# Kernel tuning notes

Measured on AMD Instinct MI355X. Metric: run time of the kernel, lower is better.

The kernel has to match this reference:

```python
import jax, jax.numpy as jnp
import numpy as np

B, T, C = 2, 2048, 1024
H = 16
D = C // H
E = 16
K = 2
THETA = 10000.0
ALPHA = 0.01
EPS = 1e-5


def rmsnorm(x, w):
    ms = jnp.mean(jnp.square(x), axis=-1, keepdims=True)
    return x * jax.lax.rsqrt(ms + EPS) * w


def rope_cos_sin(t_len, dim):
    # matches precompute_freqs_cis: freqs = theta**(-2i/dim), angles = t * freqs
    freqs = 1.0 / THETA ** (jnp.arange(0, dim // 2, dtype=jnp.float32) * 2.0 / dim)
    ang = jnp.arange(t_len, dtype=jnp.float32)[:, None] * freqs[None, :]  # [T, D/2]
    return jnp.cos(ang), jnp.sin(ang)


def apply_rope(x, cos, sin):
    # x: [B,T,H,D]; complex rotation on consecutive pairs (view_as_complex semantics)
    xr = x.reshape(x.shape[:-1] + (D // 2, 2))
    x0, x1 = xr[..., 0], xr[..., 1]
    c = cos[None, :, None, :]
    s = sin[None, :, None, :]
    return jnp.stack([x0 * c - x1 * s, x0 * s + x1 * c], axis=-1).reshape(x.shape)


def mlp(x, wf, bf, wp, bp):
    return jax.nn.silu(x @ wf + bf) @ wp + bp


def setup_inputs() -> dict:
    key = jax.random.key(0)
    ks = jax.random.split(key, 16)
    s = 0.02
    return {
        'x': jax.random.normal(ks[0], (B, T, C), jnp.float32),
        'ln1_w': jax.random.normal(ks[1], (C,), jnp.float32),
        'ln2_w': jax.random.normal(ks[2], (C,), jnp.float32),
        'w_attn': jax.random.normal(ks[3], (C, 3 * C), jnp.float32) * s,
        'b_attn': jnp.zeros((3 * C,), jnp.float32),
        'w_proj': jax.random.normal(ks[4], (C, C), jnp.float32) * s,
        'b_proj': jnp.zeros((C,), jnp.float32),
        'gate_w': jax.random.normal(ks[5], (E, C), jnp.float32) * s,
        'gate_bias': jnp.zeros((E,), jnp.float32),
        'exp_wf': jax.random.normal(ks[6], (E, C, 2 * C), jnp.float32) * s,
        'exp_bf': jnp.zeros((E, 2 * C), jnp.float32),
        'exp_wp': jax.random.normal(ks[7], (E, 2 * C, C), jnp.float32) * s,
        'exp_bp': jnp.zeros((E, C), jnp.float32),
        'sh_wf': jax.random.normal(ks[8], (C, 2 * C), jnp.float32) * s,
        'sh_bf': jnp.zeros((2 * C,), jnp.float32),
        'sh_wp': jax.random.normal(ks[9], (2 * C, C), jnp.float32) * s,
        'sh_bp': jnp.zeros((C,), jnp.float32),
    }


def reference(x, ln1_w, ln2_w, w_attn, b_attn, w_proj, b_proj, gate_w, gate_bias,
              exp_wf, exp_bf, exp_wp, exp_bp, sh_wf, sh_bf, sh_wp, sh_bp):
    # ---- attention sub-block ----
    h = rmsnorm(x, ln1_w)
    qkv = h @ w_attn + b_attn  # [B,T,3C]
    q, k, v = jnp.split(qkv, 3, axis=-1)
    q = q.reshape(B, T, H, D)
    k = k.reshape(B, T, H, D)
    v = v.reshape(B, T, H, D)
    cos, sin = rope_cos_sin(T, D)
    q = apply_rope(q, cos, sin)
    k = apply_rope(k, cos, sin)
    scores = jnp.einsum('bqhd,bkhd->bhqk', q, k) / jnp.sqrt(jnp.float32(D))
    causal = jnp.tril(jnp.ones((T, T), dtype=bool))
    scores = jnp.where(causal, scores, -jnp.inf)
    attn = jax.nn.softmax(scores, axis=-1)
    y = jnp.einsum('bhqk,bkhd->bqhd', attn, v).reshape(B, T, C)
    x = x + y @ w_proj + b_proj
    # ---- MoE sub-block ----
    h = rmsnorm(x, ln2_w).reshape(-1, C)  # [N,C]
    N = h.shape[0]
    logits = h @ gate_w.T
    p = jax.nn.softmax(logits.astype(jnp.float32), axis=-1)  # original_scores [N,E]
    _, idx = jax.lax.top_k(p + gate_bias, K)  # topk on biased scores
    w_sel = jnp.take_along_axis(p, idx, axis=-1)  # weights from unbiased scores [N,K]
    onehot = jax.nn.one_hot(idx, E, dtype=p.dtype)  # [N,K,E]
    w_dense = jnp.sum(onehot * w_sel[..., None], axis=1)  # [N,E] combine weights
    counts = jnp.sum(onehot, axis=(0, 1))  # bincount
    f_i = counts * E / (K * N + 1e-6)
    expert_probs = p.mean(axis=0)
    lb_loss = ALPHA * jnp.sum(f_i * expert_probs)
    out = jnp.zeros_like(h)
    for i in range(E):  # fixed small expert count
        out = out + mlp(h, exp_wf[i], exp_bf[i], exp_wp[i], exp_bp[i]) * w_dense[:, i:i + 1]
    out = out + mlp(h, sh_wf, sh_bf, sh_wp, sh_bp)
    return x + out.reshape(B, T, C), lb_loss
```

## Files before the change

### kernel.cpp

```cpp
#include <hip/hip_runtime.h>

typedef __bf16 bf16x8 __attribute__((ext_vector_type(8)));
typedef short  short8 __attribute__((ext_vector_type(8)));
typedef float  f32x4  __attribute__((ext_vector_type(4)));
typedef unsigned short u16;

#define NTOK 4096
#define TSEQ 2048
#define CDIM 1024
#define NEXP 16

__device__ __forceinline__ u16 f2bf(float f){
  union { float f; unsigned u; } v; v.f = f;
  unsigned r = v.u + 0x7fffu + ((v.u >> 16) & 1u);
  return (u16)(r >> 16);
}
__device__ __forceinline__ float bf2f(u16 u){
  union { unsigned u; float f; } v; v.u = ((unsigned)u) << 16; return v.f;
}

__device__ __forceinline__ f32x4 mfma16(short8 a, short8 b, f32x4 c){
  return __builtin_amdgcn_mfma_f32_16x16x32_bf16(
      __builtin_bit_cast(bf16x8, a), __builtin_bit_cast(bf16x8, b), c, 0, 0, 0);
}

__device__ __forceinline__ void gload_lds16(const void* g, void* l){
  __builtin_amdgcn_global_load_lds((__attribute__((address_space(1))) void*)g,
                                   (__attribute__((address_space(3))) void*)l,
                                   16, 0, 0);
}

__device__ __forceinline__ void tp_body(const float* __restrict__ in, u16* __restrict__ out,
                                        int K, int N, int k0, int n0, u16* lds16, int tid)
{
  int tx = tid & 15;
#pragma unroll
  for (int p = 0; p < 2; ++p) {
    int q = (tid >> 4) + p * 16;
    int k = 2 * q;
    float4 v0 = *(const float4*)(in + (size_t)(k0 + k)     * N + n0 + tx * 4);
    float4 v1 = *(const float4*)(in + (size_t)(k0 + k + 1) * N + n0 + tx * 4);
    const float* a0 = (const float*)&v0;
    const float* a1 = (const float*)&v1;
#pragma unroll
    for (int i = 0; i < 4; ++i) {
      unsigned val = (unsigned)f2bf(a0[i]) | ((unsigned)f2bf(a1[i]) << 16);
      *(unsigned*)&lds16[(tx * 4 + i) * 66 + k] = val;
    }
  }
  __syncthreads();
#pragma unroll
  for (int p = 0; p < 2; ++p) {
    int n = (tid >> 3) + p * 32;
    int k8 = (tid & 7) * 8;
    const unsigned* l32 = (const unsigned*)&lds16[n * 66 + k8];
    uint4 o4;
    o4.x = l32[0]; o4.y = l32[1]; o4.z = l32[2]; o4.w = l32[3];
    *(uint4*)(out + (size_t)(n0 + n) * K + k0 + k8) = o4;
  }
}

__global__ void transpose_wattn_k(const float* __restrict__ in, u16* __restrict__ out)
{
  __shared__ u16 lds16[64 * 66];
  int r = blockIdx.x;
  int n0 = (r % 48) * 64, k0 = (r / 48) * 64;
  tp_body(in, out, 1024, 3072, k0, n0, lds16, threadIdx.x);
}

__global__ void concat_bias_k(const float* __restrict__ exp_bf, const float* __restrict__ sh_bf,
                              const float* __restrict__ exp_bp, const float* __restrict__ sh_bp,
                              float* __restrict__ bf17, float* __restrict__ bp17,
                              int* __restrict__ counts)
{
  int i = blockIdx.x * 256 + threadIdx.x;
  if (i < 16 * 2048) bf17[i] = exp_bf[i];
  else if (i < 17 * 2048) bf17[i] = sh_bf[i - 16 * 2048];
  if (i < 16 * 1024) bp17[i] = exp_bp[i];
  else if (i < 17 * 1024) bp17[i] = sh_bp[i - 16 * 1024];
  if (blockIdx.x == 0 && threadIdx.x <= NEXP)
    counts[threadIdx.x] = (threadIdx.x == NEXP) ? NTOK : 0;
}

__global__ void rmsnorm_k(const float* __restrict__ x, const float* __restrict__ w,
                          u16* __restrict__ ob)
{
  int row = blockIdx.x, tid = threadIdx.x;
  const float4* xr = (const float4*)(x + (size_t)row * CDIM);
  float4 v = xr[tid];
  float ss = v.x*v.x + v.y*v.y + v.z*v.z + v.w*v.w;
  for (int d = 1; d < 64; d <<= 1) ss += __shfl_xor(ss, d);
  __shared__ float wacc[4];
  if ((tid & 63) == 0) wacc[tid >> 6] = ss;
  __syncthreads();
  float tot = wacc[0] + wacc[1] + wacc[2] + wacc[3];
  float scale = rsqrtf(tot * (1.0f / CDIM) + 1e-5f);
  float4 wv = ((const float4*)w)[tid];
  float o0 = v.x * scale * wv.x, o1 = v.y * scale * wv.y;
  float o2 = v.z * scale * wv.z, o3 = v.w * scale * wv.w;
  ushort4 ov; ov.x = f2bf(o0); ov.y = f2bf(o1); ov.z = f2bf(o2); ov.w = f2bf(o3);
  ((ushort4*)(ob + (size_t)row * CDIM))[tid] = ov;
}

__global__ void rmsnorm_gate_k(const float* __restrict__ x2, const float* __restrict__ w,
                               const float* __restrict__ gw, const float* __restrict__ gb,
                               u16* __restrict__ ob,
                               int* __restrict__ route_e, float* __restrict__ route_w,
                               int* __restrict__ counts, float* __restrict__ probs)
{
  int row = blockIdx.x, tid = threadIdx.x;
  __shared__ float hrow[CDIM];
  __shared__ float wacc[4];
  __shared__ float part[16][17];
  __shared__ float sm[16];

  const float4* xr = (const float4*)(x2 + (size_t)row * CDIM);
  float4 v = xr[tid];
  float ss = v.x*v.x + v.y*v.y + v.z*v.z + v.w*v.w;
  for (int d = 1; d < 64; d <<= 1) ss += __shfl_xor(ss, d);
  if ((tid & 63) == 0) wacc[tid >> 6] = ss;
  __syncthreads();
  float tot = wacc[0] + wacc[1] + wacc[2] + wacc[3];
  float scale = rsqrtf(tot * (1.0f / CDIM) + 1e-5f);
  float4 wv = ((const float4*)w)[tid];
  float o0 = v.x * scale * wv.x, o1 = v.y * scale * wv.y;
  float o2 = v.z * scale * wv.z, o3 = v.w * scale * wv.w;
  ((float4*)hrow)[tid] = make_float4(o0, o1, o2, o3);
  ushort4 ov; ov.x = f2bf(o0); ov.y = f2bf(o1); ov.z = f2bf(o2); ov.w = f2bf(o3);
  ((ushort4*)(ob + (size_t)row * CDIM))[tid] = ov;
  __syncthreads();

  int e = tid & 15, seg = tid >> 4;
  const float4* gw4 = (const float4*)(gw + (size_t)e * CDIM + seg * 64);
  const float4* hs4 = (const float4*)(hrow + seg * 64);
  float p = 0.f;
#pragma unroll
  for (int i = 0; i < 16; ++i) {
    float4 gv = gw4[i];
    float4 hv = hs4[i];
    p += hv.x * gv.x;
    p += hv.y * gv.y;
    p += hv.z * gv.z;
    p += hv.w * gv.w;
  }
  part[e][seg] = p;
  __syncthreads();
  if (tid < 16) {
    float lg = 0.f;
    for (int s = 0; s < 16; ++s) lg += part[tid][s];
    sm[tid] = lg;
  }
  __syncthreads();
  if (tid == 0) {
    float mx = sm[0];
    for (int i = 1; i < 16; ++i) mx = fmaxf(mx, sm[i]);
    float ssum = 0.f;
    for (int i = 0; i < 16; ++i) { float pe = expf(sm[i] - mx); sm[i] = pe; ssum += pe; }
    float inv = 1.0f / ssum;
    for (int i = 0; i < 16; ++i) sm[i] *= inv;
    int i1 = -1; float b1 = -1e30f;
    for (int i = 0; i < 16; ++i) { float t = sm[i] + gb[i]; if (t > b1) { b1 = t; i1 = i; } }
    int i2 = -1; float b2 = -1e30f;
    for (int i = 0; i < 16; ++i) { if (i == i1) continue; float t = sm[i] + gb[i]; if (t > b2) { b2 = t; i2 = i; } }
    route_e[2 * row] = i1; route_e[2 * row + 1] = i2;
    route_w[2 * row] = sm[i1]; route_w[2 * row + 1] = sm[i2];
    atomicAdd(&counts[i1], 1); atomicAdd(&counts[i2], 1);
  }
  __syncthreads();
  if (tid < 16) probs[(size_t)row * 16 + tid] = sm[tid];
}

template<int MODE, int SWZ>
__global__ void __launch_bounds__(256, 4)
gemm_bt(const u16* __restrict__ A, int lda,
        const u16* __restrict__ Bt, long long bStrideZ,
        const float* __restrict__ bias, int biasStrideZ,
        void* __restrict__ Cout,
        const float* __restrict__ resid,
        int M, int N, int K,
        const int* __restrict__ counts, const int* __restrict__ offsets,
        const int* __restrict__ tokA, u16* __restrict__ vtp)
{
  int cb, rb, z;
  if (SWZ) {
    int nwg = gridDim.x * gridDim.y * gridDim.z;
    int d = (blockIdx.z * gridDim.y + blockIdx.y) * gridDim.x + blockIdx.x;
    int o = (d & 7) * (nwg >> 3) + (d >> 3);
    cb = o % gridDim.x;
    int t2 = o / gridDim.x;
    rb = t2 % gridDim.y;
    z  = t2 / gridDim.y;
  } else {
    cb = blockIdx.x; rb = blockIdx.y; z = blockIdx.z;
  }

  int mLoc = M, rowBase = 0;
  if (counts) { mLoc = counts[z]; rowBase = offsets[z]; }
  if (rb * 128 >= mLoc) return;

  const u16* Bz = Bt + (size_t)z * bStrideZ;
  const float* bz = bias + (size_t)z * biasStrideZ;

  __shared__ u16 lds_a[2][128 * 32];
  __shared__ u16 lds_b[2][128 * 32];

  int tid = threadIdx.x;
  int lane = tid & 63, wave = tid >> 6;
  int wm = wave >> 1, wn = wave & 1;
  int srow = wave * 16 + (lane >> 2);
  int skel = (lane & 3) * 8;
  int r16 = lane & 15, g8 = (lane >> 4) * 8;

  size_t arow[2];
  int ncol[2];
#pragma unroll
  for (int c = 0; c < 2; ++c) {
    int rloc = rb * 128 + c * 64 + srow;
    if (rloc >= mLoc) rloc = mLoc - 1;
    int grow = rowBase + rloc;
    arow[c] = tokA ? (size_t)tokA[grow] : (size_t)grow;
    ncol[c] = cb * 128 + c * 64 + srow;
  }

  f32x4 acc[4][4] = {};

  auto stage = [&](int kt, int buf){
    int k0 = kt * 32;
#pragma unroll
    for (int c = 0; c < 2; ++c) {
      gload_lds16(A + arow[c] * lda + k0 + skel,
                  (char*)&lds_a[buf][0] + c * 4096 + wave * 1024);
      gload_lds16(Bz + (size_t)ncol[c] * K + k0 + skel,
                  (char*)&lds_b[buf][0] + c * 4096 + wave * 1024);
    }
  };

  int nkt = K >> 5;
  stage(0, 0);
  for (int kt = 0; kt < nkt; ++kt) {
    int buf = kt & 1;
    if (kt + 1 < nkt) {
      stage(kt + 1, buf ^ 1);
      asm volatile("s_waitcnt vmcnt(4)" ::: "memory");
    } else {
      asm volatile("s_waitcnt vmcnt(0)" ::: "memory");
    }
    __builtin_amdgcn_s_barrier();
    short8 af[4], bfr[4];
#pragma unroll
    for (int i = 0; i < 4; ++i) {
      af[i]  = *(const short8*)&lds_a[buf][(wm * 64 + i * 16 + r16) * 32 + g8];
      bfr[i] = *(const short8*)&lds_b[buf][(wn * 64 + i * 16 + r16) * 32 + g8];
    }
#pragma unroll
    for (int i = 0; i < 4; ++i)
#pragma unroll
      for (int j = 0; j < 4; ++j)
        acc[i][j] = mfma16(af[i], bfr[j], acc[i][j]);
    __builtin_amdgcn_s_barrier();
  }

#pragma unroll
  for (int i = 0; i < 4; ++i) {
    int rl0 = rb * 128 + wm * 64 + i * 16 + (lane >> 4) * 4;
#pragma unroll
    for (int j = 0; j < 4; ++j) {
      int col = cb * 128 + wn * 64 + j * 16 + r16;
      float bv = bz[col];
#pragma unroll
      for (int r = 0; r < 4; ++r) {
        int rl = rl0 + r;
        if (rl >= mLoc) continue;
        int grow = rowBase + rl;
        float v = acc[i][j][r] + bv;
        if (MODE == 0) {
          ((float*)Cout)[(size_t)grow * N + col] = v;
        } else if (MODE == 1) {
          ((float*)Cout)[(size_t)grow * N + col] = v + resid[(size_t)grow * N + col];
        } else if (MODE == 2) {
          float s = v * (1.0f / (1.0f + __expf(-v)));
          ((u16*)Cout)[(size_t)grow * N + col] = f2bf(s);
        } else if (MODE == 4) {
          ((u16*)Cout)[(size_t)grow * N + col] = f2bf(v);
        } else {
          if (col < 2048) {
            ((float*)Cout)[(size_t)grow * N + col] = v;
          } else {
            int c10 = col - 2048;
            int h = c10 >> 6, dd = c10 & 63;
            int b = grow >> 11, t = grow & 2047;
            vtp[((size_t)(b * 16 + h) * 64 + dd) * TSEQ + t] = f2bf(v);
          }
        }
      }
    }
  }
}

__global__ void __launch_bounds__(256, 4)
ff_tp_k(const u16* __restrict__ A, const u16* __restrict__ Wf17,
        const float* __restrict__ bf17, u16* __restrict__ hid17,
        const int* __restrict__ counts, const int* __restrict__ offsets,
        const int* __restrict__ tokA,
        const float* __restrict__ expWp, u16* __restrict__ oWp17)
{
  __shared__ union {
    struct { u16 a[2][128 * 32]; u16 b[2][128 * 32]; } g;
    u16 t[64 * 66];
  } sm;

  int u = blockIdx.x;
  if (u >= 8704) {
    int t = u - 8704;
    int z = t >> 9, r = t & 511;
    tp_body(expWp + (size_t)z * 2048 * 1024, oWp17 + (size_t)z * 2048 * 1024,
            2048, 1024, (r >> 4) * 64, (r & 15) * 64, sm.t, threadIdx.x);
    return;
  }

  const int N = 2048, K = 1024, lda = 1024;
  int cb = u & 15, t2 = u >> 4;
  int rb = t2 & 31, z = t2 >> 5;

  int mLoc = counts[z], rowBase = offsets[z];
  if (rb * 128 >= mLoc) return;

  const u16* Bz = Wf17 + (size_t)z * 2048 * 1024;
  const float* bz = bf17 + (size_t)z * 2048;

  int tid = threadIdx.x;
  int lane = tid & 63, wave = tid >> 6;
  int wm = wave >> 1, wn = wave & 1;
  int srow = wave * 16 + (lane >> 2);
  int skel = (lane & 3) * 8;
  int r16 = lane & 15, g8 = (lane >> 4) * 8;

  size_t arow[2];
  int ncol[2];
#pragma unroll
  for (int c = 0; c < 2; ++c) {
    int rloc = rb * 128 + c * 64 + srow;
    if (rloc >= mLoc) rloc = mLoc - 1;
    int grow = rowBase + rloc;
    arow[c] = (size_t)tokA[grow];
    ncol[c] = cb * 128 + c * 64 + srow;
  }

  f32x4 acc[4][4] = {};

  auto stage = [&](int kt, int buf){
    int k0 = kt * 32;
#pragma unroll
    for (int c = 0; c < 2; ++c) {
      gload_lds16(A + arow[c] * lda + k0 + skel,
                  (char*)&sm.g.a[buf][0] + c * 4096 + wave * 1024);
      gload_lds16(Bz + (size_t)ncol[c] * K + k0 + skel,
                  (char*)&sm.g.b[buf][0] + c * 4096 + wave * 1024);
    }
  };

  int nkt = K >> 5;
  stage(0, 0);
  for (int kt = 0; kt < nkt; ++kt) {
    int buf = kt & 1;
    if (kt + 1 < nkt) {
      stage(kt + 1, buf ^ 1);
      asm volatile("s_waitcnt vmcnt(4)" ::: "memory");
    } else {
      asm volatile("s_waitcnt vmcnt(0)" ::: "memory");
    }
    __builtin_amdgcn_s_barrier();
    short8 af[4], bfr[4];
#pragma unroll
    for (int i = 0; i < 4; ++i) {
      af[i]  = *(const short8*)&sm.g.a[buf][(wm * 64 + i * 16 + r16) * 32 + g8];
      bfr[i] = *(const short8*)&sm.g.b[buf][(wn * 64 + i * 16 + r16) * 32 + g8];
    }
#pragma unroll
    for (int i = 0; i < 4; ++i)
#pragma unroll
      for (int j = 0; j < 4; ++j)
        acc[i][j] = mfma16(af[i], bfr[j], acc[i][j]);
    __builtin_amdgcn_s_barrier();
  }

#pragma unroll
  for (int i = 0; i < 4; ++i) {
    int rl0 = rb * 128 + wm * 64 + i * 16 + (lane >> 4) * 4;
#pragma unroll
    for (int j = 0; j < 4; ++j) {
      int col = cb * 128 + wn * 64 + j * 16 + r16;
      float bv = bz[col];
#pragma unroll
      for (int r = 0; r < 4; ++r) {
        int rl = rl0 + r;
        if (rl >= mLoc) continue;
        int grow = rowBase + rl;
        float v = acc[i][j][r] + bv;
        float s = v * (1.0f / (1.0f + __expf(-v)));
        hid17[(size_t)grow * N + col] = f2bf(s);
      }
    }
  }
}

__global__ void __launch_bounds__(512, 4)
attn_tp_k(const u16* __restrict__ qr, const u16* __restrict__ kr,
          const u16* __restrict__ vt, u16* __restrict__ y,
          const float* __restrict__ wProj, const float* __restrict__ shWf,
          const float* __restrict__ shWp,  const float* __restrict__ expWf,
          u16* __restrict__ oProj, u16* __restrict__ oWf17, u16* __restrict__ oWp17)
{
  __shared__ union {
    struct { u16 lK[2][64 * 64]; u16 lV[2][64 * 64]; u16 plds[8][16 * 72]; } a;
    u16 t[2][64 * 66];
  } sm;

  int u = blockIdx.x;
  if (u >= 512) {
    int tid = threadIdx.x;
    int half = tid >> 8, t256 = tid & 255;
    int t = (u - 512) * 2 + half;
    const float* in; u16* out; int K, N, k0, n0;
    if (t < 8192) {
      int z = t >> 9, r = t & 511;
      in = expWf + (size_t)z * 2048 * 1024; out = oWf17 + (size_t)z * 2048 * 1024;
      K = 1024; N = 2048; n0 = (r & 31) * 64; k0 = (r >> 5) * 64;
    } else if (t < 8704) {
      int r = t - 8192;
      in = shWf; out = oWf17 + (size_t)16 * 2048 * 1024;
      K = 1024; N = 2048; n0 = (r & 31) * 64; k0 = (r >> 5) * 64;
    } else if (t < 9216) {
      int r = t - 8704;
      in = shWp; out = oWp17 + (size_t)16 * 2048 * 1024;
      K = 2048; N = 1024; n0 = (r & 15) * 64; k0 = (r >> 4) * 64;
    } else {
      int r = t - 9216;
      in = wProj; out = oProj; K = 1024; N = 1024; n0 = (r & 15) * 64; k0 = (r >> 4) * 64;
    }
    tp_body(in, out, K, N, k0, n0, &sm.t[half][0], t256);
    return;
  }

  int j  = u >> 5;
  int bh = u & 31;
  int b = bh >> 4, h = bh & 15;
  int qb = 15 - j;
  int tid = threadIdx.x;
  int wv = tid >> 6, lane = tid & 63;
  int qrow0 = qb * 128 + wv * 16;
  const u16* qbase = qr + (size_t)bh * TSEQ * 64;
  const u16* kbase = kr + (size_t)bh * TSEQ * 64;
  const u16* vbase = vt + (size_t)bh * 64 * TSEQ;

  u16* pw = &sm.a.plds[wv][0];

  int r16 = lane & 15, g = lane >> 4;

  short8 aq0 = *(const short8*)(qbase + (size_t)(qrow0 + r16) * 64 + g * 8);
  short8 aq1 = *(const short8*)(qbase + (size_t)(qrow0 + r16) * 64 + 32 + g * 8);

  int sRow = tid >> 3;
  int sColE = (((tid & 7) * 16) ^ ((sRow & 7) << 4)) >> 1;

  float m[4] = {-1e30f, -1e30f, -1e30f, -1e30f};
  float l[4] = {0.f, 0.f, 0.f, 0.f};
  f32x4 o[4] = {};

  int nt = 2 * qb + 2;

  auto stage = [&](int t, int buf){
    int kp = t * 64;
    gload_lds16(kbase + ((size_t)(kp + sRow) << 6) + sColE,
                (char*)&sm.a.lK[buf][0] + wv * 1024);
    gload_lds16(vbase + (size_t)sRow * TSEQ + kp + sColE,
                (char*)&sm.a.lV[buf][0] + wv * 1024);
  };

  auto compute = [&](int t, int buf){
    int kp = t * 64;
    f32x4 s[4];
    __builtin_amdgcn_s_setprio(1);
#pragma unroll
    for (int st = 0; st < 4; ++st) {
      int rowK = st * 16 + r16;
      int sw = (rowK & 7) << 4;
      short8 kb0 = *(const short8*)((const char*)&sm.a.lK[buf][0] + rowK * 128 + ((g * 16) ^ sw));
      short8 kb1 = *(const short8*)((const char*)&sm.a.lK[buf][0] + rowK * 128 + ((64 + g * 16) ^ sw));
      f32x4 acc = {0.f, 0.f, 0.f, 0.f};
      acc = mfma16(aq0, kb0, acc);
      acc = mfma16(aq1, kb1, acc);
      s[st] = acc;
    }
    __builtin_amdgcn_s_setprio(0);

    float sc[4];
#pragma unroll
    for (int r = 0; r < 4; ++r) {
      int qpos = qrow0 + g * 4 + r;
      float v0 = (kp + r16      <= qpos) ? s[0][r] * 0.125f : -1e30f;
      float v1 = (kp + 16 + r16 <= qpos) ? s[1][r] * 0.125f : -1e30f;
      float v2 = (kp + 32 + r16 <= qpos) ? s[2][r] * 0.125f : -1e30f;
      float v3 = (kp + 48 + r16 <= qpos) ? s[3][r] * 0.125f : -1e30f;
      float mx = fmaxf(fmaxf(v0, v1), fmaxf(v2, v3));
      for (int d = 1; d < 16; d <<= 1) mx = fmaxf(mx, __shfl_xor(mx, d));
      float mnew = fmaxf(m[r], mx);
      float e0 = __expf(v0 - mnew), e1 = __expf(v1 - mnew);
      float e2 = __expf(v2 - mnew), e3 = __expf(v3 - mnew);
      float scale = __expf(m[r] - mnew);
      float rs = (e0 + e1) + (e2 + e3);
      for (int d = 1; d < 16; d <<= 1) rs += __shfl_xor(rs, d);
      l[r] = l[r] * scale + rs;
      m[r] = mnew;
      sc[r] = scale;
      int prow = (g * 4 + r) * 72;
      pw[prow + r16]      = f2bf(e0);
      pw[prow + 16 + r16] = f2bf(e1);
      pw[prow + 32 + r16] = f2bf(e2);
      pw[prow + 48 + r16] = f2bf(e3);
    }
#pragma unroll
    for (int c = 0; c < 4; ++c) {
      f32x4 t4 = o[c];
      t4[0] *= sc[0]; t4[1] *= sc[1]; t4[2] *= sc[2]; t4[3] *= sc[3];
      o[c] = t4;
    }

    short8 pa0 = *(const short8*)&pw[r16 * 72 + g * 8];
    short8 pa1 = *(const short8*)&pw[r16 * 72 + 32 + g * 8];
    __builtin_amdgcn_s_setprio(1);
#pragma unroll
    for (int c = 0; c < 4; ++c) {
      int rowV = c * 16 + r16;
      int sw = (rowV & 7) << 4;
      short8 vb0 = *(const short8*)((const char*)&sm.a.lV[buf][0] + rowV * 128 + ((g * 16) ^ sw));
      short8 vb1 = *(const short8*)((const char*)&sm.a.lV[buf][0] + rowV * 128 + ((64 + g * 16) ^ sw));
      o[c] = mfma16(pa0, vb0, o[c]);
      o[c] = mfma16(pa1, vb1, o[c]);
    }
    __builtin_amdgcn_s_setprio(0);
  };

  stage(0, 0);
  for (int t = 0; t < nt; ++t) {
    int buf = t & 1;
    if (t + 1 < nt) {
      stage(t + 1, buf ^ 1);
      asm volatile("s_waitcnt vmcnt(2)" ::: "memory");
    } else {
      asm volatile("s_waitcnt vmcnt(0)" ::: "memory");
    }
    __builtin_amdgcn_s_barrier();
    compute(t, buf);
    __builtin_amdgcn_s_barrier();
  }

#pragma unroll
  for (int c = 0; c < 4; ++c)
#pragma unroll
    for (int r = 0; r < 4; ++r) {
      int qpos = qrow0 + g * 4 + r;
      float val = o[c][r] / l[r];
      y[((size_t)(b * TSEQ + qpos)) * CDIM + h * 64 + c * 16 + r16] = f2bf(val);
    }
}

__global__ void rope_qk_k(const float* __restrict__ qkv,
                          u16* __restrict__ qr, u16* __restrict__ kr)
{
  int flat = blockIdx.x * 256 + threadIdx.x;
  int i = flat & 31;
  int h = (flat >> 5) & 15;
  int n = flat >> 9;
  int b = n >> 11, t = n & 2047;
  const float* row = qkv + (size_t)n * 3072;
  float2 q = *(const float2*)(row + h * 64 + 2 * i);
  float2 k = *(const float2*)(row + 1024 + h * 64 + 2 * i);
  float freq = expf(-(float)i * (2.0f / 64.0f) * 9.210340371976184f);
  float ang = (float)t * freq;
  float sn, cs;
  sincosf(ang, &sn, &cs);
  float q0 = q.x * cs - q.y * sn, q1 = q.x * sn + q.y * cs;
  float k0 = k.x * cs - k.y * sn, k1 = k.x * sn + k.y * cs;
  int bh = b * 16 + h;
  size_t qoff = ((size_t)bh * TSEQ + t) * 64 + 2 * i;
  *(unsigned*)(qr + qoff) = (unsigned)f2bf(q0) | ((unsigned)f2bf(q1) << 16);
  *(unsigned*)(kr + qoff) = (unsigned)f2bf(k0) | ((unsigned)f2bf(k1) << 16);
}

__global__ void route_fin_k(const int* __restrict__ route_e, const float* __restrict__ route_w,
                            const int* __restrict__ counts, int* __restrict__ offs,
                            int* __restrict__ tok, float* __restrict__ tw, int* __restrict__ inv,
                            const float* __restrict__ probs, float* __restrict__ loss_out)
{
  __shared__ int curs[16];
  __shared__ float part[256][16];
  __shared__ float colsum[16];
  int tid = threadIdx.x;
  if (tid == 0) {
    int acc = 0;
    for (int e = 0; e < NEXP; ++e) { offs[e] = acc; curs[e] = acc; acc += counts[e]; }
    offs[NEXP] = acc;
  }
  __syncthreads();
  for (int n = tid; n < NTOK; n += 1024) {
    for (int j = 0; j < 2; ++j) {
      int e = route_e[2 * n + j];
      int pos = atomicAdd(&curs[e], 1);
      tok[pos] = n; tw[pos] = route_w[2 * n + j];
      inv[2 * n + j] = pos;
    }
    tok[2 * NTOK + n] = n;
  }
  __syncthreads();
  if (tid < 256) {
    float acc[16];
#pragma unroll
    for (int e = 0; e < 16; ++e) acc[e] = 0.f;
    for (int n = tid; n < NTOK; n += 256) {
      const float4* row = (const float4*)(probs + (size_t)n * 16);
      float4 a0 = row[0], a1 = row[1], a2 = row[2], a3 = row[3];
      acc[0] += a0.x; acc[1] += a0.y; acc[2]  += a0.z; acc[3]  += a0.w;
      acc[4] += a1.x; acc[5] += a1.y; acc[6]  += a1.z; acc[7]  += a1.w;
      acc[8] += a2.x; acc[9] += a2.y; acc[10] += a2.z; acc[11] += a2.w;
      acc[12] += a3.x; acc[13] += a3.y; acc[14] += a3.z; acc[15] += a3.w;
    }
#pragma unroll
    for (int e = 0; e < 16; ++e) part[tid][e] = acc[e];
  }
  __syncthreads();
  if (tid < 16) {
    float s = 0.f;
    for (int i = 0; i < 256; ++i) s += part[i][tid];
    colsum[tid] = s;
  }
  __syncthreads();
  if (tid == 0) {
    float accl = 0.f;
    for (int e = 0; e < NEXP; ++e) {
      float f = (float)counts[e] * (16.0f / (2.0f * (float)NTOK + 1e-6f));
      accl += f * (colsum[e] * (1.0f / (float)NTOK));
    }
    loss_out[0] = 0.01f * accl;
  }
}

__global__ void combine_k(float* __restrict__ out, const float* __restrict__ x2,
                          const u16* __restrict__ eout,
                          const int* __restrict__ inv, const float* __restrict__ tw)
{
  int n = blockIdx.x, tid = threadIdx.x;
  int p0 = inv[2 * n], p1 = inv[2 * n + 1];
  float w0 = tw[p0], w1 = tw[p1];
  float4 xr = ((const float4*)(x2 + (size_t)n * CDIM))[tid];
  ushort4 es = ((const ushort4*)(eout + (size_t)(2 * NTOK + n) * CDIM))[tid];
  float4 a;
  a.x = xr.x + bf2f(es.x);
  a.y = xr.y + bf2f(es.y);
  a.z = xr.z + bf2f(es.z);
  a.w = xr.w + bf2f(es.w);
  ushort4 e0 = ((const ushort4*)(eout + (size_t)p0 * CDIM))[tid];
  ushort4 e1 = ((const ushort4*)(eout + (size_t)p1 * CDIM))[tid];
  a.x += bf2f(e0.x) * w0 + bf2f(e1.x) * w1;
  a.y += bf2f(e0.y) * w0 + bf2f(e1.y) * w1;
  a.z += bf2f(e0.z) * w0 + bf2f(e1.z) * w1;
  a.w += bf2f(e0.w) * w0 + bf2f(e1.w) * w1;
  ((float4*)(out + (size_t)n * CDIM))[tid] = a;
}

extern "C" void kernel_launch(void* const* d_in, const int* in_sizes, int n_in,
                              void* d_out, int out_size, void* d_ws, size_t ws_size,
                              hipStream_t stream)
{
  const float* x      = (const float*)d_in[0];
  const float* ln1_w  = (const float*)d_in[1];
  const float* ln2_w  = (const float*)d_in[2];
  const float* w_attn = (const float*)d_in[3];
  const float* b_attn = (const float*)d_in[4];
  const float* w_proj = (const float*)d_in[5];
  const float* b_proj = (const float*)d_in[6];
  const float* gate_w = (const float*)d_in[7];
  const float* gate_b = (const float*)d_in[8];
  const float* exp_wf = (const float*)d_in[9];
  const float* exp_bf = (const float*)d_in[10];
  const float* exp_wp = (const float*)d_in[11];
  const float* exp_bp = (const float*)d_in[12];
  const float* sh_wf  = (const float*)d_in[13];
  const float* sh_bf  = (const float*)d_in[14];
  const float* sh_wp  = (const float*)d_in[15];
  const float* sh_bp  = (const float*)d_in[16];

  char* ws = (char*)d_ws;
  size_t off = 0;
  auto alloc = [&](size_t b){ size_t r = off; off = (off + b + 255) & ~(size_t)255; return r; };

  size_t oWAttnT = alloc(3072ull * 1024 * 2);
  size_t oWProjT = alloc(1024ull * 1024 * 2);
  size_t oExpWfT = alloc(17ull * 2048 * 1024 * 2);
  size_t oExpWpT = alloc(17ull * 1024 * 2048 * 2);
  size_t oX2     = alloc(4096ull * 1024 * 4);
  size_t oH2B    = alloc(4096ull * 1024 * 2);
  size_t oQKV    = alloc(4096ull * 3072 * 4);
  size_t oQR     = alloc(4096ull * 1024 * 2);
  size_t oKR     = alloc(4096ull * 1024 * 2);
  size_t oVT     = alloc(4096ull * 1024 * 2);
  size_t oH1B    = alloc(4096ull * 1024 * 2);
  size_t oCnt    = alloc(128);
  size_t oOffs   = alloc(128);
  size_t oRE     = alloc(8192ull * 4);
  size_t oRW     = alloc(8192ull * 4);
  size_t oTok    = alloc(12288ull * 4);
  size_t oTw     = alloc(8192ull * 4);
  size_t oInv    = alloc(8192ull * 4);
  size_t oProbs  = alloc(4096ull * 16 * 4);
  size_t oBf17   = alloc(17ull * 2048 * 4);
  size_t oBp17   = alloc(17ull * 1024 * 4);

  u16* pWAttnT = (u16*)(ws + oWAttnT);
  u16* pWProjT = (u16*)(ws + oWProjT);
  u16* pWf17   = (u16*)(ws + oExpWfT);
  u16* pWp17   = (u16*)(ws + oExpWpT);
  float* pX2   = (float*)(ws + oX2);
  u16* pH2B    = (u16*)(ws + oH2B);
  float* pQKV  = (float*)(ws + oQKV);
  u16* pHid17  = (u16*)(ws + oQKV);
  u16* pQR     = (u16*)(ws + oQR);
  u16* pKR     = (u16*)(ws + oKR);
  u16* pVT     = (u16*)(ws + oVT);
  u16* pH1B    = (u16*)(ws + oH1B);
  u16* pY      = (u16*)(ws + oH1B);
  u16* pEoutB  = (u16*)(ws + oQR);
  int* pCnt    = (int*)(ws + oCnt);
  int* pOffs   = (int*)(ws + oOffs);
  int* pRE     = (int*)(ws + oRE);
  float* pRW   = (float*)(ws + oRW);
  int* pTok    = (int*)(ws + oTok);
  float* pTw   = (float*)(ws + oTw);
  int* pInv    = (int*)(ws + oInv);
  float* pProbs= (float*)(ws + oProbs);
  float* pBf17 = (float*)(ws + oBf17);
  float* pBp17 = (float*)(ws + oBp17);

  transpose_wattn_k<<<768, 256, 0, stream>>>(w_attn, pWAttnT);
  concat_bias_k<<<(17 * 2048 + 255) / 256, 256, 0, stream>>>(exp_bf, sh_bf, exp_bp, sh_bp,
                                                             pBf17, pBp17, pCnt);

  rmsnorm_k<<<NTOK, 256, 0, stream>>>(x, ln1_w, pH1B);

  gemm_bt<5, 1><<<dim3(3072/128, NTOK/128, 1), 256, 0, stream>>>(
      pH1B, 1024, pWAttnT, 0, b_attn, 0, pQKV, nullptr,
      NTOK, 3072, 1024, nullptr, nullptr, nullptr, pVT);

  rope_qk_k<<<(NTOK * 16 * 32) / 256, 256, 0, stream>>>(pQKV, pQR, pKR);

  attn_tp_k<<<512 + 4736, 512, 0, stream>>>(pQR, pKR, pVT, pY,
                                            w_proj, sh_wf, sh_wp, exp_wf,
                                            pWProjT, pWf17, pWp17);

  gemm_bt<1, 1><<<dim3(1024/128, NTOK/128, 1), 256, 0, stream>>>(
      pY, 1024, pWProjT, 0, b_proj, 0, pX2, x,
      NTOK, 1024, 1024, nullptr, nullptr, nullptr, nullptr);

  rmsnorm_gate_k<<<NTOK, 256, 0, stream>>>(pX2, ln2_w, gate_w, gate_b,
                                           pH2B, pRE, pRW, pCnt, pProbs);

  route_fin_k<<<1, 1024, 0, stream>>>(pRE, pRW, pCnt, pOffs, pTok, pTw, pInv,
                                      pProbs, ((float*)d_out) + (size_t)NTOK * CDIM);

  ff_tp_k<<<8704 + 8192, 256, 0, stream>>>(pH2B, pWf17, pBf17, pHid17,
                                           pCnt, pOffs, pTok, exp_wp, pWp17);

  gemm_bt<4, 0><<<dim3(1024/128, NTOK/128, 17), 256, 0, stream>>>(
      pHid17, 2048, pWp17, 2048ll * 1024, pBp17, 1024, pEoutB, nullptr,
      NTOK, 1024, 2048, pCnt, pOffs, nullptr, nullptr);

  combine_k<<<NTOK, 256, 0, stream>>>((float*)d_out, pX2, pEoutB, pInv, pTw);

  (void)in_sizes; (void)n_in; (void)out_size; (void)ws_size;
}
```

Baseline: 555.7 us.

## Fuse fp32 expert weight conversion into MoE GEMM B-tile loads

```diff
diff --git a/kernel.cpp b/kernel.cpp
--- a/kernel.cpp
+++ b/kernel.cpp
@@ -273,15 +273,8 @@
         if (rl >= mLoc) continue;
         int grow = rowBase + rl;
         float v = acc[i][j][r] + bv;
-        if (MODE == 0) {
-          ((float*)Cout)[(size_t)grow * N + col] = v;
-        } else if (MODE == 1) {
+        if (MODE == 1) {
           ((float*)Cout)[(size_t)grow * N + col] = v + resid[(size_t)grow * N + col];
-        } else if (MODE == 2) {
-          float s = v * (1.0f / (1.0f + __expf(-v)));
-          ((u16*)Cout)[(size_t)grow * N + col] = f2bf(s);
-        } else if (MODE == 4) {
-          ((u16*)Cout)[(size_t)grow * N + col] = f2bf(v);
         } else {
           if (col < 2048) {
             ((float*)Cout)[(size_t)grow * N + col] = v;
@@ -297,36 +290,26 @@
   }
 }
 
+template<int MODE>
 __global__ void __launch_bounds__(256, 4)
-ff_tp_k(const u16* __restrict__ A, const u16* __restrict__ Wf17,
-        const float* __restrict__ bf17, u16* __restrict__ hid17,
-        const int* __restrict__ counts, const int* __restrict__ offsets,
-        const int* __restrict__ tokA,
-        const float* __restrict__ expWp, u16* __restrict__ oWp17)
-{
-  __shared__ union {
-    struct { u16 a[2][128 * 32]; u16 b[2][128 * 32]; } g;
-    u16 t[64 * 66];
-  } sm;
-
-  int u = blockIdx.x;
-  if (u >= 8704) {
-    int t = u - 8704;
-    int z = t >> 9, r = t & 511;
-    tp_body(expWp + (size_t)z * 2048 * 1024, oWp17 + (size_t)z * 2048 * 1024,
-            2048, 1024, (r >> 4) * 64, (r & 15) * 64, sm.t, threadIdx.x);
-    return;
-  }
-
-  const int N = 2048, K = 1024, lda = 1024;
-  int cb = u & 15, t2 = u >> 4;
-  int rb = t2 & 31, z = t2 >> 5;
+moe_gemm(const u16* __restrict__ A, int lda,
+         const float* __restrict__ expW, const float* __restrict__ shW,
+         long long wStrideZ,
+         const float* __restrict__ bias17, int biasStride,
+         u16* __restrict__ out, int N, int K,
+         const int* __restrict__ counts, const int* __restrict__ offsets,
+         const int* __restrict__ tokA)
+{
+  int cb = blockIdx.x, rb = blockIdx.y, z = blockIdx.z;
 
   int mLoc = counts[z], rowBase = offsets[z];
   if (rb * 128 >= mLoc) return;
 
-  const u16* Bz = Wf17 + (size_t)z * 2048 * 1024;
-  const float* bz = bf17 + (size_t)z * 2048;
+  const float* Wz = (z == 16) ? shW : (expW + (size_t)z * wStrideZ);
+  const float* bz = bias17 + (size_t)z * biasStride;
+
+  __shared__ u16 lds_a[2][128 * 32];
+  __shared__ u16 lds_b[2][128 * 40];
 
   int tid = threadIdx.x;
   int lane = tid & 63, wave = tid >> 6;
@@ -335,53 +318,63 @@
   int skel = (lane & 3) * 8;
   int r16 = lane & 15, g8 = (lane >> 4) * 8;
 
+  int kp = tid >> 4;
+  int nbase = tid & 15;
+  const float* wRow0base = Wz + (size_t)(cb * 128 + nbase);
+
   size_t arow[2];
-  int ncol[2];
 #pragma unroll
   for (int c = 0; c < 2; ++c) {
     int rloc = rb * 128 + c * 64 + srow;
     if (rloc >= mLoc) rloc = mLoc - 1;
     int grow = rowBase + rloc;
-    arow[c] = (size_t)tokA[grow];
-    ncol[c] = cb * 128 + c * 64 + srow;
+    arow[c] = tokA ? (size_t)tokA[grow] : (size_t)grow;
   }
 
   f32x4 acc[4][4] = {};
 
-  auto stage = [&](int kt, int buf){
+  auto stageA = [&](int kt, int buf){
     int k0 = kt * 32;
 #pragma unroll
-    for (int c = 0; c < 2; ++c) {
+    for (int c = 0; c < 2; ++c)
       gload_lds16(A + arow[c] * lda + k0 + skel,
-                  (char*)&sm.g.a[buf][0] + c * 4096 + wave * 1024);
-      gload_lds16(Bz + (size_t)ncol[c] * K + k0 + skel,
-                  (char*)&sm.g.b[buf][0] + c * 4096 + wave * 1024);
-    }
+                  (char*)&lds_a[buf][0] + c * 4096 + wave * 1024);
   };
+  float w0[8], w1[8];
+  auto loadB = [&](int kt){
+    const float* r0 = wRow0base + (size_t)(kt * 32 + 2 * kp) * N;
+    const float* r1 = r0 + N;
+#pragma unroll
+    for (int j = 0; j < 8; ++j) { w0[j] = r0[16 * j]; w1[j] = r1[16 * j]; }
+  };
+  auto writeB = [&](int buf){
+#pragma unroll
+    for (int j = 0; j < 8; ++j) {
+      unsigned val = (unsigned)f2bf(w0[j]) | ((unsigned)f2bf(w1[j]) << 16);
+      *(unsigned*)&lds_b[buf][(nbase + 16 * j) * 40 + 2 * kp] = val;
+    }
+  };
 
   int nkt = K >> 5;
-  stage(0, 0);
+  loadB(0); stageA(0, 0); writeB(0);
+  __syncthreads();
+
   for (int kt = 0; kt < nkt; ++kt) {
     int buf = kt & 1;
-    if (kt + 1 < nkt) {
-      stage(kt + 1, buf ^ 1);
-      asm volatile("s_waitcnt vmcnt(4)" ::: "memory");
-    } else {
-      asm volatile("s_waitcnt vmcnt(0)" ::: "memory");
-    }
-    __builtin_amdgcn_s_barrier();
+    if (kt + 1 < nkt) { loadB(kt + 1); stageA(kt + 1, buf ^ 1); }
     short8 af[4], bfr[4];
 #pragma unroll
     for (int i = 0; i < 4; ++i) {
-      af[i]  = *(const short8*)&sm.g.a[buf][(wm * 64 + i * 16 + r16) * 32 + g8];
-      bfr[i] = *(const short8*)&sm.g.b[buf][(wn * 64 + i * 16 + r16) * 32 + g8];
+      af[i]  = *(const short8*)&lds_a[buf][(wm * 64 + i * 16 + r16) * 32 + g8];
+      bfr[i] = *(const short8*)&lds_b[buf][(wn * 64 + i * 16 + r16) * 40 + g8];
     }
 #pragma unroll
     for (int i = 0; i < 4; ++i)
 #pragma unroll
       for (int j = 0; j < 4; ++j)
         acc[i][j] = mfma16(af[i], bfr[j], acc[i][j]);
-    __builtin_amdgcn_s_barrier();
+    if (kt + 1 < nkt) writeB(buf ^ 1);
+    __syncthreads();
   }
 
 #pragma unroll
@@ -397,8 +390,12 @@
         if (rl >= mLoc) continue;
         int grow = rowBase + rl;
         float v = acc[i][j][r] + bv;
-        float s = v * (1.0f / (1.0f + __expf(-v)));
-        hid17[(size_t)grow * N + col] = f2bf(s);
+        if (MODE == 2) {
+          float s = v * (1.0f / (1.0f + __expf(-v)));
+          out[(size_t)grow * N + col] = f2bf(s);
+        } else {
+          out[(size_t)grow * N + col] = f2bf(v);
+        }
       }
     }
   }
@@ -407,9 +404,7 @@
 __global__ void __launch_bounds__(512, 4)
 attn_tp_k(const u16* __restrict__ qr, const u16* __restrict__ kr,
           const u16* __restrict__ vt, u16* __restrict__ y,
-          const float* __restrict__ wProj, const float* __restrict__ shWf,
-          const float* __restrict__ shWp,  const float* __restrict__ expWf,
-          u16* __restrict__ oProj, u16* __restrict__ oWf17, u16* __restrict__ oWp17)
+          const float* __restrict__ wProj, u16* __restrict__ oProj)
 {
   __shared__ union {
     struct { u16 lK[2][64 * 64]; u16 lV[2][64 * 64]; u16 plds[8][16 * 72]; } a;
@@ -421,24 +416,8 @@
     int tid = threadIdx.x;
     int half = tid >> 8, t256 = tid & 255;
     int t = (u - 512) * 2 + half;
-    const float* in; u16* out; int K, N, k0, n0;
-    if (t < 8192) {
-      int z = t >> 9, r = t & 511;
-      in = expWf + (size_t)z * 2048 * 1024; out = oWf17 + (size_t)z * 2048 * 1024;
-      K = 1024; N = 2048; n0 = (r & 31) * 64; k0 = (r >> 5) * 64;
-    } else if (t < 8704) {
-      int r = t - 8192;
-      in = shWf; out = oWf17 + (size_t)16 * 2048 * 1024;
-      K = 1024; N = 2048; n0 = (r & 31) * 64; k0 = (r >> 5) * 64;
-    } else if (t < 9216) {
-      int r = t - 8704;
-      in = shWp; out = oWp17 + (size_t)16 * 2048 * 1024;
-      K = 2048; N = 1024; n0 = (r & 15) * 64; k0 = (r >> 4) * 64;
-    } else {
-      int r = t - 9216;
-      in = wProj; out = oProj; K = 1024; N = 1024; n0 = (r & 15) * 64; k0 = (r >> 4) * 64;
-    }
-    tp_body(in, out, K, N, k0, n0, &sm.t[half][0], t256);
+    int n0 = (t & 15) * 64, k0 = (t >> 4) * 64;
+    tp_body(wProj, oProj, 1024, 1024, k0, n0, &sm.t[half][0], t256);
     return;
   }
 
@@ -470,15 +449,15 @@
   int nt = 2 * qb + 2;
 
   auto stage = [&](int t, int buf){
-    int kp = t * 64;
-    gload_lds16(kbase + ((size_t)(kp + sRow) << 6) + sColE,
+    int kp2 = t * 64;
+    gload_lds16(kbase + ((size_t)(kp2 + sRow) << 6) + sColE,
                 (char*)&sm.a.lK[buf][0] + wv * 1024);
-    gload_lds16(vbase + (size_t)sRow * TSEQ + kp + sColE,
+    gload_lds16(vbase + (size_t)sRow * TSEQ + kp2 + sColE,
                 (char*)&sm.a.lV[buf][0] + wv * 1024);
   };
 
   auto compute = [&](int t, int buf){
-    int kp = t * 64;
+    int kp2 = t * 64;
     f32x4 s[4];
     __builtin_amdgcn_s_setprio(1);
 #pragma unroll
@@ -498,10 +477,10 @@
 #pragma unroll
     for (int r = 0; r < 4; ++r) {
       int qpos = qrow0 + g * 4 + r;
-      float v0 = (kp + r16      <= qpos) ? s[0][r] * 0.125f : -1e30f;
-      float v1 = (kp + 16 + r16 <= qpos) ? s[1][r] * 0.125f : -1e30f;
-      float v2 = (kp + 32 + r16 <= qpos) ? s[2][r] * 0.125f : -1e30f;
-      float v3 = (kp + 48 + r16 <= qpos) ? s[3][r] * 0.125f : -1e30f;
+      float v0 = (kp2 + r16      <= qpos) ? s[0][r] * 0.125f : -1e30f;
+      float v1 = (kp2 + 16 + r16 <= qpos) ? s[1][r] * 0.125f : -1e30f;
+      float v2 = (kp2 + 32 + r16 <= qpos) ? s[2][r] * 0.125f : -1e30f;
+      float v3 = (kp2 + 48 + r16 <= qpos) ? s[3][r] * 0.125f : -1e30f;
       float mx = fmaxf(fmaxf(v0, v1), fmaxf(v2, v3));
       for (int d = 1; d < 16; d <<= 1) mx = fmaxf(mx, __shfl_xor(mx, d));
       float mnew = fmaxf(m[r], mx);
@@ -696,8 +675,6 @@
 
   size_t oWAttnT = alloc(3072ull * 1024 * 2);
   size_t oWProjT = alloc(1024ull * 1024 * 2);
-  size_t oExpWfT = alloc(17ull * 2048 * 1024 * 2);
-  size_t oExpWpT = alloc(17ull * 1024 * 2048 * 2);
   size_t oX2     = alloc(4096ull * 1024 * 4);
   size_t oH2B    = alloc(4096ull * 1024 * 2);
   size_t oQKV    = alloc(4096ull * 3072 * 4);
@@ -718,8 +695,6 @@
 
   u16* pWAttnT = (u16*)(ws + oWAttnT);
   u16* pWProjT = (u16*)(ws + oWProjT);
-  u16* pWf17   = (u16*)(ws + oExpWfT);
-  u16* pWp17   = (u16*)(ws + oExpWpT);
   float* pX2   = (float*)(ws + oX2);
   u16* pH2B    = (u16*)(ws + oH2B);
   float* pQKV  = (float*)(ws + oQKV);
@@ -753,9 +728,7 @@
 
   rope_qk_k<<<(NTOK * 16 * 32) / 256, 256, 0, stream>>>(pQKV, pQR, pKR);
 
-  attn_tp_k<<<512 + 4736, 512, 0, stream>>>(pQR, pKR, pVT, pY,
-                                            w_proj, sh_wf, sh_wp, exp_wf,
-                                            pWProjT, pWf17, pWp17);
+  attn_tp_k<<<512 + 128, 512, 0, stream>>>(pQR, pKR, pVT, pY, w_proj, pWProjT);
 
   gemm_bt<1, 1><<<dim3(1024/128, NTOK/128, 1), 256, 0, stream>>>(
       pY, 1024, pWProjT, 0, b_proj, 0, pX2, x,
@@ -767,12 +740,13 @@
   route_fin_k<<<1, 1024, 0, stream>>>(pRE, pRW, pCnt, pOffs, pTok, pTw, pInv,
                                       pProbs, ((float*)d_out) + (size_t)NTOK * CDIM);
 
-  ff_tp_k<<<8704 + 8192, 256, 0, stream>>>(pH2B, pWf17, pBf17, pHid17,
-                                           pCnt, pOffs, pTok, exp_wp, pWp17);
-
-  gemm_bt<4, 0><<<dim3(1024/128, NTOK/128, 17), 256, 0, stream>>>(
-      pHid17, 2048, pWp17, 2048ll * 1024, pBp17, 1024, pEoutB, nullptr,
-      NTOK, 1024, 2048, pCnt, pOffs, nullptr, nullptr);
+  moe_gemm<2><<<dim3(2048/128, NTOK/128, 17), 256, 0, stream>>>(
+      pH2B, 1024, exp_wf, sh_wf, 2048ll * 1024, pBf17, 2048, pHid17,
+      2048, 1024, pCnt, pOffs, pTok);
+
+  moe_gemm<4><<<dim3(1024/128, NTOK/128, 17), 256, 0, stream>>>(
+      pHid17, 2048, exp_wp, sh_wp, 2048ll * 1024, pBp17, 1024, pEoutB,
+      1024, 2048, pCnt, pOffs, nullptr);
 
   combine_k<<<NTOK, 256, 0, stream>>>((float*)d_out, pX2, pEoutB, pInv, pTw);
 
```

New measurement: 566.9 us. +2.0%, slower.
